# Performance work log

Measured on AMD Instinct MI355X. Metric: run time of the kernel, lower is better.

The kernel has to match this reference:

```python
import jax, jax.numpy as jnp
import numpy as np
import math

B, S, H, NH = 2, 2048, 1024, 16
DK = H // NH


def setup_inputs() -> dict:
    key = jax.random.key(0)
    k1, k2, k3 = jax.random.split(key, 3)
    scale = 1.0 / math.sqrt(H)
    return {
        "x": jax.random.normal(k1, (B, S, H), dtype=jnp.float32),
        "w_attn": jax.random.normal(k2, (H, 3 * H), dtype=jnp.float32) * scale,
        "b_attn": jnp.zeros((3 * H,), dtype=jnp.float32),
        "w_proj": jax.random.normal(k3, (H, H), dtype=jnp.float32) * scale,
        "b_proj": jnp.zeros((H,), dtype=jnp.float32),
    }


def reference(x, w_attn, b_attn, w_proj, b_proj):
    bs, seq_len, hidden = x.shape
    qkv = x @ w_attn + b_attn                       # [B,S,3H]
    q, k, v = jnp.split(qkv, 3, axis=-1)
    # [B,S,H] -> [B,NH,S,DK]
    def heads(t):
        return t.reshape(bs, seq_len, NH, DK).transpose(0, 2, 1, 3)
    q, k, v = heads(q), heads(k), heads(v)
    scores = jnp.einsum('bhqd,bhkd->bhqk', q, k) / math.sqrt(DK)  # [B,NH,S,S]
    causal = jnp.tril(jnp.ones((seq_len, seq_len), dtype=bool))
    scores = jnp.where(causal[None, None], scores, -jnp.inf)
    attn = jax.nn.softmax(scores, axis=-1)
    out = jnp.einsum('bhqk,bhkd->bhqd', attn, v)    # [B,NH,S,DK]
    out = out.transpose(0, 2, 1, 3).reshape(bs, seq_len, hidden)
    return out @ w_proj + b_proj
```

## Files before the change

### kernel.cpp

```cpp
#include <hip/hip_runtime.h>

#define BATCH 2
#define S_LEN 2048
#define NHEADS 16
#define DKV 64
#define HID 1024

typedef __attribute__((ext_vector_type(8))) short s16x8;
typedef __attribute__((ext_vector_type(4))) short s16x4;
typedef __attribute__((ext_vector_type(4))) float f32x4;

__device__ inline unsigned short f2bf(float f) {
    union { float f; unsigned int u; } v; v.f = f;
    unsigned int r = v.u + 0x7fffu + ((v.u >> 16) & 1u);
    return (unsigned short)(r >> 16);
}

__device__ inline s16x8 pack8(float4 a, float4 b) {
    s16x8 r;
    r[0] = (short)f2bf(a.x); r[1] = (short)f2bf(a.y);
    r[2] = (short)f2bf(a.z); r[3] = (short)f2bf(a.w);
    r[4] = (short)f2bf(b.x); r[5] = (short)f2bf(b.y);
    r[6] = (short)f2bf(b.z); r[7] = (short)f2bf(b.w);
    return r;
}

__device__ inline void gload_lds16(const void* g, void* l) {
    __builtin_amdgcn_global_load_lds(
        (const __attribute__((address_space(1))) void*)g,
        (__attribute__((address_space(3))) void*)l, 16, 0, 0);
}

__device__ inline unsigned int cvtpk_bf16(float lo, float hi) {
    unsigned int d;
    asm("v_cvt_pk_bf16_f32 %0, %1, %2" : "=v"(d) : "v"(lo), "v"(hi));
    return d;
}

__global__ __launch_bounds__(256)
void f32_to_bf16_kernel(const float* __restrict__ in, unsigned short* __restrict__ out, int n8) {
    int i = blockIdx.x * 256 + threadIdx.x;
    if (i < n8) {
        const float4* p = (const float4*)(in + (size_t)i * 8);
        float4 a = p[0], b = p[1];
        *(s16x8*)(out + (size_t)i * 8) = pack8(a, b);
    }
}

__global__ __launch_bounds__(256)
void transpose_bf16_kernel(const float* __restrict__ in, unsigned short* __restrict__ out,
                           int K, int N) {
    __shared__ float tile[32][33];
    int n0 = blockIdx.x * 32;
    int k0 = blockIdx.y * 32;
    int tx = threadIdx.x, ty = threadIdx.y;
    for (int i = ty; i < 32; i += 8)
        tile[i][tx] = in[(size_t)(k0 + i) * N + n0 + tx];
    __syncthreads();
    for (int i = ty; i < 32; i += 8)
        out[(size_t)(n0 + i) * K + k0 + tx] = f2bf(tile[tx][i]);
}

__global__ __launch_bounds__(256)
void gemm_qkv_kernel(const unsigned short* __restrict__ A, const unsigned short* __restrict__ Bt,
                     const float* __restrict__ bias, unsigned short* __restrict__ qkv,
                     unsigned short* __restrict__ vT, int M, int N, int K) {
    __shared__ __align__(16) unsigned short As[2][128 * 32];
    __shared__ __align__(16) unsigned short Bs[2][128 * 32];

    const int tid  = threadIdx.x;
    const int lane = tid & 63;
    const int wv   = tid >> 6;
    const int wr   = wv >> 1, wc = wv & 1;

    const int wg  = blockIdx.x;
    const int xcd = wg & 7;
    const int idx = wg >> 3;
    const int m0  = (idx & 31) * 128;
    const int n0  = (xcd * 3 + (idx >> 5)) * 128;

    const int lr = lane & 15;
    const int lg = lane >> 4;
    const int lk = lg * 8;

    const int srow = lane >> 2;
    const int scol = (lane & 3) * 8;

    f32x4 acc[4][4] = {};
    int cur = 0;

    #pragma unroll
    for (int l = 0; l < 2; l++) {
        const int r0 = wv * 32 + l * 16;
        gload_lds16(A  + (size_t)(m0 + r0 + srow) * K + scol, &As[0][r0 * 32]);
        gload_lds16(Bt + (size_t)(n0 + r0 + srow) * K + scol, &Bs[0][r0 * 32]);
    }

    for (int k0 = 0; k0 < K; k0 += 32) {
        __syncthreads();

        if (k0 + 32 < K) {
            #pragma unroll
            for (int l = 0; l < 2; l++) {
                const int r0 = wv * 32 + l * 16;
                gload_lds16(A  + (size_t)(m0 + r0 + srow) * K + k0 + 32 + scol, &As[cur ^ 1][r0 * 32]);
                gload_lds16(Bt + (size_t)(n0 + r0 + srow) * K + k0 + 32 + scol, &Bs[cur ^ 1][r0 * 32]);
            }
        }

        s16x8 af[4], bfr[4];
        #pragma unroll
        for (int mi = 0; mi < 4; mi++)
            af[mi] = *(const s16x8*)&As[cur][(wr * 64 + mi * 16 + lr) * 32 + lk];
        #pragma unroll
        for (int ni = 0; ni < 4; ni++)
            bfr[ni] = *(const s16x8*)&Bs[cur][(wc * 64 + ni * 16 + lr) * 32 + lk];
        #pragma unroll
        for (int mi = 0; mi < 4; mi++)
            #pragma unroll
            for (int ni = 0; ni < 4; ni++)
                acc[mi][ni] = __builtin_amdgcn_mfma_f32_16x16x32_bf16(af[mi], bfr[ni], acc[mi][ni], 0, 0, 0);
        cur ^= 1;
    }

    const bool isV = (n0 >= 2 * HID);
    #pragma unroll
    for (int mi = 0; mi < 4; mi++) {
        #pragma unroll
        for (int ni = 0; ni < 4; ni++) {
            int col = n0 + wc * 64 + ni * 16 + lr;
            float bv = bias[col];
            int row0 = m0 + wr * 64 + mi * 16 + lg * 4;
            if (isV) {
                int d = col - 2 * HID;
                int bb = row0 >> 11;
                int s = row0 & (S_LEN - 1);
                int sl = s & 63;
                int sp = (sl & 0x23) | ((sl & 0x10) >> 2) | ((sl & 0x0C) << 1);
                int sc = (s & ~63) | sp;
                s16x4 pk;
                #pragma unroll
                for (int r = 0; r < 4; r++)
                    pk[r] = (short)f2bf(acc[mi][ni][r] + bv);
                *(s16x4*)&vT[((size_t)bb * HID + d) * S_LEN + sc] = pk;
            } else {
                #pragma unroll
                for (int r = 0; r < 4; r++)
                    qkv[(size_t)(row0 + r) * (2 * HID) + col] = f2bf(acc[mi][ni][r] + bv);
            }
        }
    }
}

__global__ __launch_bounds__(256)
void gemm64_kernel(const unsigned short* __restrict__ A, const unsigned short* __restrict__ Bt,
                   const float* __restrict__ bias, float* __restrict__ Cout,
                   int M, int N, int K) {
    __shared__ __align__(16) unsigned short As[2][64 * 32];
    __shared__ __align__(16) unsigned short Bs[2][128 * 32];

    const int tid  = threadIdx.x;
    const int lane = tid & 63;
    const int wv   = tid >> 6;
    const int wr   = wv >> 1, wc = wv & 1;
    const int m0   = blockIdx.y * 64, n0 = blockIdx.x * 128;

    const int lr = lane & 15;
    const int lg = lane >> 4;
    const int lk = lg * 8;

    const int srow = lane >> 2;
    const int scol = (lane & 3) * 8;

    const int arow = tid >> 2;
    const int acol = (tid & 3) * 8;

    f32x4 acc[2][4] = {};
    int cur = 0;

    gload_lds16(A + (size_t)(m0 + arow) * K + acol, &As[0][(arow & ~3) * 32]);
    #pragma unroll
    for (int l = 0; l < 2; l++) {
        const int r0 = wv * 32 + l * 16;
        gload_lds16(Bt + (size_t)(n0 + r0 + srow) * K + scol, &Bs[0][r0 * 32]);
    }

    for (int k0 = 0; k0 < K; k0 += 32) {
        __syncthreads();

        if (k0 + 32 < K) {
            gload_lds16(A + (size_t)(m0 + arow) * K + k0 + 32 + acol, &As[cur ^ 1][(arow & ~3) * 32]);
            #pragma unroll
            for (int l = 0; l < 2; l++) {
                const int r0 = wv * 32 + l * 16;
                gload_lds16(Bt + (size_t)(n0 + r0 + srow) * K + k0 + 32 + scol, &Bs[cur ^ 1][r0 * 32]);
            }
        }

        s16x8 af[2], bfr[4];
        #pragma unroll
        for (int mi = 0; mi < 2; mi++)
            af[mi] = *(const s16x8*)&As[cur][(wr * 32 + mi * 16 + lr) * 32 + lk];
        #pragma unroll
        for (int ni = 0; ni < 4; ni++)
            bfr[ni] = *(const s16x8*)&Bs[cur][(wc * 64 + ni * 16 + lr) * 32 + lk];
        #pragma unroll
        for (int mi = 0; mi < 2; mi++)
            #pragma unroll
            for (int ni = 0; ni < 4; ni++)
                acc[mi][ni] = __builtin_amdgcn_mfma_f32_16x16x32_bf16(af[mi], bfr[ni], acc[mi][ni], 0, 0, 0);
        cur ^= 1;
    }

    #pragma unroll
    for (int mi = 0; mi < 2; mi++) {
        #pragma unroll
        for (int ni = 0; ni < 4; ni++) {
            int col = n0 + wc * 64 + ni * 16 + lr;
            float bv = bias[col];
            #pragma unroll
            for (int r = 0; r < 4; r++) {
                int row = m0 + wr * 32 + mi * 16 + lg * 4 + r;
                Cout[(size_t)row * N + col] = acc[mi][ni][r] + bv;
            }
        }
    }
}

__global__ __launch_bounds__(512)
void attn_kernel(const unsigned short* __restrict__ qkv, const unsigned short* __restrict__ vT,
                 unsigned short* __restrict__ out) {
    __shared__ __align__(16) unsigned short Ks[2][2][64 * 64];
    __shared__ __align__(16) unsigned short Vs[2][2][64 * 64];

    const int tid  = threadIdx.x;
    const int lane = tid & 63;
    const int wv   = tid >> 6;
    const int grp  = wv >> 2;
    const int w    = wv & 3;

    const int wgid = blockIdx.x;
    const int xcd  = wgid & 7;
    const int slot = wgid >> 3;
    const int pp   = slot & 15;
    const int g    = (slot >> 4) * 8 + xcd;
    const int head = g & 15;
    const int b    = g >> 4;

    const size_t rowbase = (size_t)b * S_LEN;
    const int hoff = head * DKV;

    const int lr = lane & 15;
    const int lg = lane >> 4;
    const int lk = lg * 8;

    const int krow   = lane >> 3;
    const int kchunk = ((lane & 7) ^ krow) * 8;

    float* scratch = (float*)&Ks[0][0][0];

    #pragma unroll
    for (int panel = 0; panel < 2; panel++) {
        const int qb = (panel == 0) ? pp : (31 - pp);
        const int q0 = qb * 64;
        const int niter = (qb + 2) >> 1;

        s16x8 qf[2];
        {
            const unsigned short* qp = qkv + (rowbase + q0 + w * 16 + lr) * (2 * HID) + hoff;
            qf[0] = *(const s16x8*)(qp + lk);
            qf[1] = *(const s16x8*)(qp + 32 + lk);
        }

        f32x4 o[4] = {};
        float lsum = 0.0f;
        int cur = 0;

        __syncthreads();
        if (grp <= qb) {
            const int j0 = grp * 64;
            #pragma unroll
            for (int l = 0; l < 2; l++) {
                const int r0 = (w * 2 + l) * 8;
                gload_lds16(qkv + (rowbase + j0 + r0 + krow) * (2 * HID) + HID + hoff + kchunk,
                            &Ks[grp][0][r0 * 64]);
                gload_lds16(vT + ((size_t)b * HID + hoff + r0 + krow) * S_LEN + j0 + kchunk,
                            &Vs[grp][0][r0 * 64]);
            }
        }

        for (int it = 0; it < niter; it++) {
            const int t = 2 * it + grp;
            __syncthreads();

            if (t + 2 <= qb) {
                const int jn = (t + 2) * 64;
                #pragma unroll
                for (int l = 0; l < 2; l++) {
                    const int r0 = (w * 2 + l) * 8;
                    gload_lds16(qkv + (rowbase + jn + r0 + krow) * (2 * HID) + HID + hoff + kchunk,
                                &Ks[grp][cur ^ 1][r0 * 64]);
                    gload_lds16(vT + ((size_t)b * HID + hoff + r0 + krow) * S_LEN + jn + kchunk,
                                &Vs[grp][cur ^ 1][r0 * 64]);
                }
            }

            if (t <= qb) {
                f32x4 sfT[4] = {};
                #pragma unroll
                for (int kt = 0; kt < 2; kt++)
                    #pragma unroll
                    for (int ni = 0; ni < 4; ni++) {
                        s16x8 kb = *(const s16x8*)&Ks[grp][cur][(ni * 16 + lr) * 64 + (((kt * 4 + lg) ^ (lr & 7)) * 8)];
                        sfT[ni] = __builtin_amdgcn_mfma_f32_16x16x32_bf16(kb, qf[kt], sfT[ni], 0, 0, 0);
                    }

                const bool diag = (t == qb);
                unsigned int own[4][2];
                #pragma unroll
                for (int ni = 0; ni < 4; ni++) {
                    float pv[4];
                    #pragma unroll
                    for (int r = 0; r < 4; r++) {
                        float s = sfT[ni][r];
                        if (diag) {
                            int kl = ni * 16 + lg * 4 + r;
                            if (kl > w * 16 + lr) s = -INFINITY;
                        }
                        pv[r] = exp2f(__fmaf_rn(s, 0.18033688f, -17.3123405f));
                    }
                    lsum += (pv[0] + pv[1]) + (pv[2] + pv[3]);
                    own[ni][0] = cvtpk_bf16(pv[0], pv[1]);
                    own[ni][1] = cvtpk_bf16(pv[2], pv[3]);
                }

                #pragma unroll
                for (int kt = 0; kt < 2; kt++) {
                    union { unsigned int u[4]; s16x8 v; } pa;
                    pa.u[0] = own[2 * kt][0];
                    pa.u[1] = own[2 * kt][1];
                    pa.u[2] = own[2 * kt + 1][0];
                    pa.u[3] = own[2 * kt + 1][1];
                    #pragma unroll
                    for (int dt = 0; dt < 4; dt++) {
                        s16x8 vb = *(const s16x8*)&Vs[grp][cur][(dt * 16 + lr) * 64 + (((kt * 4 + lg) ^ (lr & 7)) * 8)];
                        o[dt] = __builtin_amdgcn_mfma_f32_16x16x32_bf16(vb, pa.v, o[dt], 0, 0, 0);
                    }
                }
            }
            cur ^= 1;
        }

        __syncthreads();
        const int sbase = (w * 64 + lane) * 17;
        if (grp == 1) {
            #pragma unroll
            for (int dt = 0; dt < 4; dt++)
                #pragma unroll
                for (int r = 0; r < 4; r++)
                    scratch[sbase + dt * 4 + r] = o[dt][r];
            scratch[sbase + 16] = lsum;
        }
        __syncthreads();
        if (grp == 0) {
            #pragma unroll
            for (int dt = 0; dt < 4; dt++)
                #pragma unroll
                for (int r = 0; r < 4; r++)
                    o[dt][r] += scratch[sbase + dt * 4 + r];
            lsum += scratch[sbase + 16];
            lsum += __shfl_xor(lsum, 16, 64);
            lsum += __shfl_xor(lsum, 32, 64);
            float invl = 1.0f / lsum;
            int qrow = q0 + w * 16 + lr;
            #pragma unroll
            for (int dt = 0; dt < 4; dt++) {
                s16x4 pk;
                #pragma unroll
                for (int r = 0; r < 4; r++) pk[r] = (short)f2bf(o[dt][r] * invl);
                *(s16x4*)&out[(rowbase + qrow) * HID + hoff + dt * 16 + lg * 4] = pk;
            }
        }
    }
}

extern "C" void kernel_launch(void* const* d_in, const int* in_sizes, int n_in,
                              void* d_out, int out_size, void* d_ws, size_t ws_size,
                              hipStream_t stream) {
    const float* x      = (const float*)d_in[0];
    const float* w_attn = (const float*)d_in[1];
    const float* b_attn = (const float*)d_in[2];
    const float* w_proj = (const float*)d_in[3];
    const float* b_proj = (const float*)d_in[4];
    float* out = (float*)d_out;

    char* ws = (char*)d_ws;
    unsigned short* qkv      = (unsigned short*)(ws);
    unsigned short* waT      = (unsigned short*)(ws + 16777216);
    unsigned short* wpT      = (unsigned short*)(ws + 23068672);
    unsigned short* attn_out = (unsigned short*)(ws + 25165824);
    unsigned short* xb       = (unsigned short*)(ws + 33554432);
    unsigned short* vTr      = (unsigned short*)(ws + 41943040);

    const int M = BATCH * S_LEN;

    f32_to_bf16_kernel<<<dim3((M * HID / 8 + 255) / 256), 256, 0, stream>>>(x, xb, M * HID / 8);

    dim3 tb(32, 8);
    transpose_bf16_kernel<<<dim3(3 * HID / 32, HID / 32), tb, 0, stream>>>(w_attn, waT, HID, 3 * HID);
    transpose_bf16_kernel<<<dim3(HID / 32, HID / 32), tb, 0, stream>>>(w_proj, wpT, HID, HID);

    gemm_qkv_kernel<<<dim3(768), 256, 0, stream>>>(
        xb, waT, b_attn, qkv, vTr, M, 3 * HID, HID);

    attn_kernel<<<dim3(512), 512, 0, stream>>>(qkv, vTr, attn_out);

    gemm64_kernel<<<dim3(HID / 128, M / 64), 256, 0, stream>>>(
        attn_out, wpT, b_proj, out, M, HID, HID);
}
```

Measured before the change: 118.3 us.

## Fuse input prep kernels, drop XCD-aware QKV tile mapping, add MFMA priority hints

```diff
diff --git a/kernel.cpp b/kernel.cpp
--- a/kernel.cpp
+++ b/kernel.cpp
@@ -38,27 +38,41 @@
 }
 
 __global__ __launch_bounds__(256)
-void f32_to_bf16_kernel(const float* __restrict__ in, unsigned short* __restrict__ out, int n8) {
-    int i = blockIdx.x * 256 + threadIdx.x;
-    if (i < n8) {
-        const float4* p = (const float4*)(in + (size_t)i * 8);
+void prep_kernel(const float* __restrict__ x, unsigned short* __restrict__ xb,
+                 const float* __restrict__ w_attn, unsigned short* __restrict__ waT,
+                 const float* __restrict__ w_proj, unsigned short* __restrict__ wpT) {
+    __shared__ float tile[32][33];
+    const int blk = blockIdx.x;
+    const int tid = threadIdx.x;
+
+    if (blk < 2048) {
+        int i = blk * 256 + tid;
+        const float4* p = (const float4*)(x + (size_t)i * 8);
         float4 a = p[0], b = p[1];
-        *(s16x8*)(out + (size_t)i * 8) = pack8(a, b);
-    }
-}
-
-__global__ __launch_bounds__(256)
-void transpose_bf16_kernel(const float* __restrict__ in, unsigned short* __restrict__ out,
-                           int K, int N) {
-    __shared__ float tile[32][33];
-    int n0 = blockIdx.x * 32;
-    int k0 = blockIdx.y * 32;
-    int tx = threadIdx.x, ty = threadIdx.y;
+        *(s16x8*)(xb + (size_t)i * 8) = pack8(a, b);
+        return;
+    }
+
+    const float* in;
+    unsigned short* outp;
+    int n0, k0, N;
+    if (blk < 5120) {
+        int idx = blk - 2048;
+        N = 3 * HID;
+        n0 = (idx % 96) * 32; k0 = (idx / 96) * 32;
+        in = w_attn; outp = waT;
+    } else {
+        int idx = blk - 5120;
+        N = HID;
+        n0 = (idx % 32) * 32; k0 = (idx / 32) * 32;
+        in = w_proj; outp = wpT;
+    }
+    const int tx = tid & 31, ty = tid >> 5;
     for (int i = ty; i < 32; i += 8)
         tile[i][tx] = in[(size_t)(k0 + i) * N + n0 + tx];
     __syncthreads();
     for (int i = ty; i < 32; i += 8)
-        out[(size_t)(n0 + i) * K + k0 + tx] = f2bf(tile[tx][i]);
+        outp[(size_t)(n0 + i) * HID + k0 + tx] = f2bf(tile[tx][i]);
 }
 
 __global__ __launch_bounds__(256)
@@ -72,12 +86,7 @@
     const int lane = tid & 63;
     const int wv   = tid >> 6;
     const int wr   = wv >> 1, wc = wv & 1;
-
-    const int wg  = blockIdx.x;
-    const int xcd = wg & 7;
-    const int idx = wg >> 3;
-    const int m0  = (idx & 31) * 128;
-    const int n0  = (xcd * 3 + (idx >> 5)) * 128;
+    const int m0   = blockIdx.y * 128, n0 = blockIdx.x * 128;
 
     const int lr = lane & 15;
     const int lg = lane >> 4;
@@ -307,6 +316,7 @@
 
             if (t <= qb) {
                 f32x4 sfT[4] = {};
+                __builtin_amdgcn_s_setprio(1);
                 #pragma unroll
                 for (int kt = 0; kt < 2; kt++)
                     #pragma unroll
@@ -314,6 +324,7 @@
                         s16x8 kb = *(const s16x8*)&Ks[grp][cur][(ni * 16 + lr) * 64 + (((kt * 4 + lg) ^ (lr & 7)) * 8)];
                         sfT[ni] = __builtin_amdgcn_mfma_f32_16x16x32_bf16(kb, qf[kt], sfT[ni], 0, 0, 0);
                     }
+                __builtin_amdgcn_s_setprio(0);
 
                 const bool diag = (t == qb);
                 unsigned int own[4][2];
@@ -334,6 +345,7 @@
                     own[ni][1] = cvtpk_bf16(pv[2], pv[3]);
                 }
 
+                __builtin_amdgcn_s_setprio(1);
                 #pragma unroll
                 for (int kt = 0; kt < 2; kt++) {
                     union { unsigned int u[4]; s16x8 v; } pa;
@@ -347,6 +359,7 @@
                         o[dt] = __builtin_amdgcn_mfma_f32_16x16x32_bf16(vb, pa.v, o[dt], 0, 0, 0);
                     }
                 }
+                __builtin_amdgcn_s_setprio(0);
             }
             cur ^= 1;
         }
@@ -404,13 +417,9 @@
 
     const int M = BATCH * S_LEN;
 
-    f32_to_bf16_kernel<<<dim3((M * HID / 8 + 255) / 256), 256, 0, stream>>>(x, xb, M * HID / 8);
-
-    dim3 tb(32, 8);
-    transpose_bf16_kernel<<<dim3(3 * HID / 32, HID / 32), tb, 0, stream>>>(w_attn, waT, HID, 3 * HID);
-    transpose_bf16_kernel<<<dim3(HID / 32, HID / 32), tb, 0, stream>>>(w_proj, wpT, HID, HID);
-
-    gemm_qkv_kernel<<<dim3(768), 256, 0, stream>>>(
+    prep_kernel<<<dim3(6144), 256, 0, stream>>>(x, xb, w_attn, waT, w_proj, wpT);
+
+    gemm_qkv_kernel<<<dim3(3 * HID / 128, M / 128), 256, 0, stream>>>(
         xb, waT, b_attn, qkv, vTr, M, 3 * HID, HID);
 
     attn_kernel<<<dim3(512), 512, 0, stream>>>(qkv, vTr, attn_out);
```

After: 108.9 us. 8.0% less time.
